# Optimization experiments

Hardware: AMD Instinct MI355X
Metric: run time of the kernel (lower is better)

Reference implementation:

```python
import jax, jax.numpy as jnp
import numpy as np

M, H, D, P = 16, 32, 128, 8192
N = H * D


def setup_inputs() -> dict:
    key = jax.random.key(0)
    k1, k2, k3, k4, k5, k6 = jax.random.split(key, 6)
    X = jax.random.normal(k1, (M, N), dtype=jnp.float32)
    # small init scale keeps the module's naive (unstabilized) exp-softmax finite
    Wq = jax.random.normal(k2, (N, N), dtype=jnp.float32) * 0.02
    Wk = jax.random.normal(k3, (N, N), dtype=jnp.float32) * 0.02
    Wv = jax.random.normal(k4, (N, N), dtype=jnp.float32) * 0.02
    cache_K = jax.random.normal(k5, (H, P, D), dtype=jnp.float32) * 0.05
    cache_V = jax.random.normal(k6, (H, P, D), dtype=jnp.float32)
    return {"X": X, "Wq": Wq, "Wk": Wk, "Wv": Wv,
            "cache_K": cache_K, "cache_V": cache_V}


def reference(X, Wq, Wk, Wv, cache_K, cache_V):
    m, n = X.shape                      # [M, N]
    h, p, d = cache_K.shape             # [H, P, D]
    # RMSNorm (no learned scale, matches (X*X).sum / N)
    x2 = jnp.sum(X * X, axis=1)
    x_norm = X / jnp.sqrt(x2 / n)[:, None]
    # QKV projections (nn.Linear, no bias -> x @ W.T)
    q = (x_norm @ Wq.T).reshape(m, h, d).transpose(1, 0, 2)   # [H, M, D]
    k = (x_norm @ Wk.T).reshape(m, h, d).transpose(1, 0, 2)   # [H, M, D]
    v = (x_norm @ Wv.T).reshape(m, h, d).transpose(1, 0, 2)   # [H, M, D]
    # append to cache
    ck = jnp.concatenate([cache_K, k], axis=1)                # [H, P+M, D]
    cv = jnp.concatenate([cache_V, v], axis=1)                # [H, P+M, D]
    # scores (no 1/sqrt(D) scaling in the original) + naive softmax
    c = jnp.einsum('hmd,hpd->hmp', q, ck)                     # [H, M, P+M]
    c_exp = jnp.exp(c)
    c_div = c_exp / jnp.sum(c_exp, axis=2, keepdims=True)
    o = jnp.einsum('hmp,hpd->hmd', c_div, cv)                 # [H, M, D]
    return o.transpose(1, 0, 2).reshape(m, n)                 # [M, N]
```

## Files before the change

### kernel.cpp

```cpp
#include <hip/hip_runtime.h>

#define NN 4096
#define HH 32
#define DD 128
#define MM 16
#define PP 8192

__device__ __forceinline__ float4 ld4(const float* p) { return *(const float4*)p; }
__device__ __forceinline__ float dot4f(float4 a, float4 b) {
  return a.x * b.x + a.y * b.y + a.z * b.z + a.w * b.w;
}
__device__ __forceinline__ void accumv(float* o, float e, float4 a, float4 b,
                                       float4 c, float4 d) {
  o[0] += e * a.x;  o[1] += e * a.y;  o[2] += e * a.z;  o[3] += e * a.w;
  o[4] += e * b.x;  o[5] += e * b.y;  o[6] += e * b.z;  o[7] += e * b.w;
  o[8] += e * c.x;  o[9] += e * c.y;  o[10] += e * c.z; o[11] += e * c.w;
  o[12] += e * d.x; o[13] += e * d.y; o[14] += e * d.z; o[15] += e * d.w;
}

__global__ void k1_rms(const float* __restrict__ X, float* __restrict__ inv) {
  const int m = blockIdx.x;
  const int tid = threadIdx.x;
  float s = 0.f;
#pragma unroll
  for (int i = 0; i < 16; ++i) {
    float v = X[(size_t)m * NN + i * 256 + tid];
    s += v * v;
  }
#pragma unroll
  for (int off = 1; off < 64; off <<= 1) s += __shfl_xor(s, off, 64);
  __shared__ float red[4];
  if ((tid & 63) == 0) red[tid >> 6] = s;
  __syncthreads();
  if (tid == 0) {
    float t = red[0] + red[1] + red[2] + red[3];
    inv[m] = rsqrtf(t * (1.0f / (float)NN));
  }
}

__global__ __launch_bounds__(256, 4) void k2_qkv(
    const float* __restrict__ X, const float* __restrict__ Wq,
    const float* __restrict__ Wk, const float* __restrict__ Wv,
    float* __restrict__ c_part) {
  __shared__ float lds_c[4][32][18];
  const int b = blockIdx.x;
  const int mat = b >> 9;
  const int rem = b & 511;
  const int qt = rem >> 7;
  const int jg = rem & 127;
  const float* W = (mat == 0) ? Wq : (mat == 1) ? Wk : Wv;
  const int tid = threadIdx.x;
  const int wave = tid >> 6;
  const int lane = tid & 63;
  const int m4 = lane & 3;
  const int g = lane >> 2;
  const int kbase = qt * 1024 + wave * 256 + g * 16;

  float4 xr[4][4];
#pragma unroll
  for (int mi = 0; mi < 4; ++mi) {
    const float* xp = X + (size_t)(mi * 4 + m4) * NN + kbase;
#pragma unroll
    for (int j = 0; j < 4; ++j) xr[mi][j] = ld4(xp + j * 4);
  }

  const int j0 = jg * 32;
  for (int grp = 0; grp < 8; ++grp) {
    float acc[4][4];
#pragma unroll
    for (int r = 0; r < 4; ++r)
#pragma unroll
      for (int mi = 0; mi < 4; ++mi) acc[r][mi] = 0.f;
#pragma unroll
    for (int r = 0; r < 4; ++r) {
      const float* wp = W + (size_t)(j0 + grp * 4 + r) * NN + kbase;
      float4 w0 = ld4(wp);
      float4 w1 = ld4(wp + 4);
      float4 w2 = ld4(wp + 8);
      float4 w3 = ld4(wp + 12);
#pragma unroll
      for (int mi = 0; mi < 4; ++mi)
        acc[r][mi] = acc[r][mi] + dot4f(xr[mi][0], w0) + dot4f(xr[mi][1], w1) +
                     dot4f(xr[mi][2], w2) + dot4f(xr[mi][3], w3);
    }
#pragma unroll
    for (int off = 4; off < 64; off <<= 1)
#pragma unroll
      for (int r = 0; r < 4; ++r)
#pragma unroll
        for (int mi = 0; mi < 4; ++mi)
          acc[r][mi] += __shfl_xor(acc[r][mi], off, 64);
    if (g == 0) {
#pragma unroll
      for (int r = 0; r < 4; ++r)
#pragma unroll
        for (int mi = 0; mi < 4; ++mi)
          lds_c[wave][grp * 4 + r][mi * 4 + m4] = acc[r][mi];
    }
  }
  __syncthreads();
#pragma unroll
  for (int i = 0; i < 2; ++i) {
    const int idx = i * 256 + tid;
    const int j = idx & 31;
    const int m = idx >> 5;
    float s = lds_c[0][j][m] + lds_c[1][j][m] + lds_c[2][j][m] + lds_c[3][j][m];
    c_part[(((size_t)(mat * 4 + qt) * 16 + m) << 12) + (j0 + j)] = s;
  }
}

__global__ __launch_bounds__(256, 4) void k3_attn(
    const float* __restrict__ cK, const float* __restrict__ cV,
    const float* __restrict__ c_part, const float* __restrict__ inv,
    float* __restrict__ o_part, float* __restrict__ denom_part) {
  const int chunk = blockIdx.x;
  const int h = blockIdx.y;
  const int tid = threadIdx.x;
  const int wave = tid >> 6;
  const int lane = tid & 63;
  const int m8 = lane & 7;
  const int g = lane >> 3;
  const int d0 = g * 16;

  float4 qa[4], qb[4];
  {
    float f[2][16];
#pragma unroll
    for (int mi = 0; mi < 2; ++mi)
#pragma unroll
      for (int j = 0; j < 16; ++j) f[mi][j] = 0.f;
#pragma unroll
    for (int qt = 0; qt < 4; ++qt) {
#pragma unroll
      for (int mi = 0; mi < 2; ++mi) {
        const int m = mi * 8 + m8;
        const float* cp = c_part + (((size_t)(qt * 16 + m)) << 12) + h * DD + d0;
#pragma unroll
        for (int j = 0; j < 4; ++j) {
          float4 t = ld4(cp + j * 4);
          f[mi][j * 4 + 0] += t.x;
          f[mi][j * 4 + 1] += t.y;
          f[mi][j * 4 + 2] += t.z;
          f[mi][j * 4 + 3] += t.w;
        }
      }
    }
    const float i0 = inv[m8];
    const float i1 = inv[8 + m8];
#pragma unroll
    for (int j = 0; j < 4; ++j) {
      qa[j] = make_float4(f[0][j * 4] * i0, f[0][j * 4 + 1] * i0,
                          f[0][j * 4 + 2] * i0, f[0][j * 4 + 3] * i0);
      qb[j] = make_float4(f[1][j * 4] * i1, f[1][j * 4 + 1] * i1,
                          f[1][j * 4 + 2] * i1, f[1][j * 4 + 3] * i1);
    }
  }

  float oac0[16], oac1[16];
#pragma unroll
  for (int j = 0; j < 16; ++j) { oac0[j] = 0.f; oac1[j] = 0.f; }
  float den0 = 0.f, den1 = 0.f;

  if (chunk < 32) {
    const size_t rowb = ((size_t)h * PP + chunk * 256 + wave * 64) * DD;
    const float* kb = cK + rowb + d0;
    const float* vb = cV + rowb + d0;
#pragma unroll 2
    for (int pi = 0; pi < 64; ++pi) {
      const float* kp = kb + pi * DD;
      float4 k0 = ld4(kp), k1 = ld4(kp + 4), k2 = ld4(kp + 8), k3 = ld4(kp + 12);
      const float* vp = vb + pi * DD;
      float4 v0 = ld4(vp), v1 = ld4(vp + 4), v2 = ld4(vp + 8), v3 = ld4(vp + 12);
      float c0 = dot4f(qa[0], k0) + dot4f(qa[1], k1) + dot4f(qa[2], k2) + dot4f(qa[3], k3);
      float c1 = dot4f(qb[0], k0) + dot4f(qb[1], k1) + dot4f(qb[2], k2) + dot4f(qb[3], k3);
#pragma unroll
      for (int off = 8; off < 64; off <<= 1) {
        c0 += __shfl_xor(c0, off, 64);
        c1 += __shfl_xor(c1, off, 64);
      }
      float e0 = __expf(c0), e1 = __expf(c1);
      den0 += e0; den1 += e1;
      accumv(oac0, e0, v0, v1, v2, v3);
      accumv(oac1, e1, v0, v1, v2, v3);
    }
  } else {
#pragma unroll
    for (int pi = 0; pi < 4; ++pi) {
      const int p = wave * 4 + pi;
      float kk[16], vv[16];
#pragma unroll
      for (int j = 0; j < 16; ++j) { kk[j] = 0.f; vv[j] = 0.f; }
#pragma unroll
      for (int qt = 0; qt < 4; ++qt) {
        const float* cpk = c_part + (((size_t)((4 + qt) * 16 + p)) << 12) + h * DD + d0;
        const float* cpv = c_part + (((size_t)((8 + qt) * 16 + p)) << 12) + h * DD + d0;
#pragma unroll
        for (int j = 0; j < 4; ++j) {
          float4 tk = ld4(cpk + j * 4);
          float4 tv = ld4(cpv + j * 4);
          kk[j * 4 + 0] += tk.x; kk[j * 4 + 1] += tk.y;
          kk[j * 4 + 2] += tk.z; kk[j * 4 + 3] += tk.w;
          vv[j * 4 + 0] += tv.x; vv[j * 4 + 1] += tv.y;
          vv[j * 4 + 2] += tv.z; vv[j * 4 + 3] += tv.w;
        }
      }
      const float ip = inv[p];
      float4 k0 = make_float4(kk[0] * ip, kk[1] * ip, kk[2] * ip, kk[3] * ip);
      float4 k1 = make_float4(kk[4] * ip, kk[5] * ip, kk[6] * ip, kk[7] * ip);
      float4 k2 = make_float4(kk[8] * ip, kk[9] * ip, kk[10] * ip, kk[11] * ip);
      float4 k3 = make_float4(kk[12] * ip, kk[13] * ip, kk[14] * ip, kk[15] * ip);
      float4 v0 = make_float4(vv[0] * ip, vv[1] * ip, vv[2] * ip, vv[3] * ip);
      float4 v1 = make_float4(vv[4] * ip, vv[5] * ip, vv[6] * ip, vv[7] * ip);
      float4 v2 = make_float4(vv[8] * ip, vv[9] * ip, vv[10] * ip, vv[11] * ip);
      float4 v3 = make_float4(vv[12] * ip, vv[13] * ip, vv[14] * ip, vv[15] * ip);
      float c0 = dot4f(qa[0], k0) + dot4f(qa[1], k1) + dot4f(qa[2], k2) + dot4f(qa[3], k3);
      float c1 = dot4f(qb[0], k0) + dot4f(qb[1], k1) + dot4f(qb[2], k2) + dot4f(qb[3], k3);
#pragma unroll
      for (int off = 8; off < 64; off <<= 1) {
        c0 += __shfl_xor(c0, off, 64);
        c1 += __shfl_xor(c1, off, 64);
      }
      float e0 = __expf(c0), e1 = __expf(c1);
      den0 += e0; den1 += e1;
      accumv(oac0, e0, v0, v1, v2, v3);
      accumv(oac1, e1, v0, v1, v2, v3);
    }
  }

  const size_t wc = ((size_t)h * 33 + chunk) * 4 + wave;
  float* op0 = o_part + wc * 2048 + m8 * DD + d0;
  float* op1 = o_part + wc * 2048 + (8 + m8) * DD + d0;
#pragma unroll
  for (int j = 0; j < 4; ++j) {
    *(float4*)(op0 + j * 4) = make_float4(oac0[j * 4], oac0[j * 4 + 1],
                                          oac0[j * 4 + 2], oac0[j * 4 + 3]);
    *(float4*)(op1 + j * 4) = make_float4(oac1[j * 4], oac1[j * 4 + 1],
                                          oac1[j * 4 + 2], oac1[j * 4 + 3]);
  }
  if (g == 0) {
    denom_part[wc * 16 + m8] = den0;
    denom_part[wc * 16 + 8 + m8] = den1;
  }
}

__global__ void k4_final(const float* __restrict__ o_part,
                         const float* __restrict__ denom_part,
                         float* __restrict__ out) {
  const int b = blockIdx.x;
  const int h = b >> 3;
  const int sub = b & 7;
  const int tid = threadIdx.x;
  const int md = sub * 256 + tid;
  __shared__ float dinv[2];
  if (tid == 0 || tid == 128) {
    const int mm = md >> 7;
    float s = 0.f;
    for (int c = 0; c < 132; ++c)
      s += denom_part[((size_t)h * 132 + c) * 16 + mm];
    dinv[tid >> 7] = 1.0f / s;
  }
  __syncthreads();
  float s = 0.f;
  for (int c = 0; c < 132; ++c)
    s += o_part[((size_t)h * 132 + c) * 2048 + md];
  const int m = md >> 7;
  const int d = md & 127;
  out[(size_t)m * NN + h * DD + d] = s * dinv[tid >> 7];
}

extern "C" void kernel_launch(void* const* d_in, const int* in_sizes, int n_in,
                              void* d_out, int out_size, void* d_ws, size_t ws_size,
                              hipStream_t stream) {
  (void)in_sizes; (void)n_in; (void)out_size; (void)ws_size;
  const float* X  = (const float*)d_in[0];
  const float* Wq = (const float*)d_in[1];
  const float* Wk = (const float*)d_in[2];
  const float* Wv = (const float*)d_in[3];
  const float* cK = (const float*)d_in[4];
  const float* cV = (const float*)d_in[5];
  float* out = (float*)d_out;
  float* ws = (float*)d_ws;

  float* inv        = ws;
  float* c_part     = ws + 16;
  float* o_part     = c_part + 786432;
  float* denom_part = o_part + 8650752;

  k1_rms<<<16, 256, 0, stream>>>(X, inv);
  k2_qkv<<<1536, 256, 0, stream>>>(X, Wq, Wk, Wv, c_part);
  k3_attn<<<dim3(33, 32), 256, 0, stream>>>(cK, cV, c_part, inv, o_part, denom_part);
  k4_final<<<256, 256, 0, stream>>>(o_part, denom_part, out);
}
```

Baseline: 537.1 us.

## Stage weights and KV cache through double-buffered LDS, add QKV combine kernel

The QKV projection now cooperatively loads contiguous 4-row weight tiles into double-buffered shared memory with register prefetch, instead of each lane issuing strided global loads. A new combine kernel sums the split-K partials and applies the RMS scale once, so the attention kernel no longer recomputes q/k/v from partials in every block. Attention is regridded to 512 blocks of 512 positions each, with K/V tiles staged through double-buffered LDS and the new-token tail folded into one block per head. The cost is an extra launch, more barriers and lower occupancy from the larger LDS footprint.

```diff
diff --git a/kernel.cpp b/kernel.cpp
--- a/kernel.cpp
+++ b/kernel.cpp
@@ -6,16 +6,9 @@
 #define MM 16
 #define PP 8192
 
-__device__ __forceinline__ float4 ld4(const float* p) { return *(const float4*)p; }
+__device__ __forceinline__ float4 ld4(const float* p) { return *(const float4*)(p); }
 __device__ __forceinline__ float dot4f(float4 a, float4 b) {
   return a.x * b.x + a.y * b.y + a.z * b.z + a.w * b.w;
-}
-__device__ __forceinline__ void accumv(float* o, float e, float4 a, float4 b,
-                                       float4 c, float4 d) {
-  o[0] += e * a.x;  o[1] += e * a.y;  o[2] += e * a.z;  o[3] += e * a.w;
-  o[4] += e * b.x;  o[5] += e * b.y;  o[6] += e * b.z;  o[7] += e * b.w;
-  o[8] += e * c.x;  o[9] += e * c.y;  o[10] += e * c.z; o[11] += e * c.w;
-  o[12] += e * d.x; o[13] += e * d.y; o[14] += e * d.z; o[15] += e * d.w;
 }
 
 __global__ void k1_rms(const float* __restrict__ X, float* __restrict__ inv) {
@@ -38,23 +31,24 @@
   }
 }
 
-__global__ __launch_bounds__(256, 4) void k2_qkv(
+__global__ __launch_bounds__(256, 3) void k2_qkv(
     const float* __restrict__ X, const float* __restrict__ Wq,
     const float* __restrict__ Wk, const float* __restrict__ Wv,
     float* __restrict__ c_part) {
-  __shared__ float lds_c[4][32][18];
+  __shared__ float wt[2][4][1024];
+  __shared__ float lds_c[4][32][17];
   const int b = blockIdx.x;
   const int mat = b >> 9;
-  const int rem = b & 511;
-  const int qt = rem >> 7;
-  const int jg = rem & 127;
+  const int qt = (b >> 7) & 3;
+  const int rb = b & 127;
   const float* W = (mat == 0) ? Wq : (mat == 1) ? Wk : Wv;
   const int tid = threadIdx.x;
   const int wave = tid >> 6;
   const int lane = tid & 63;
   const int m4 = lane & 3;
   const int g = lane >> 2;
-  const int kbase = qt * 1024 + wave * 256 + g * 16;
+  const int kwin = wave * 256 + g * 16;
+  const int kbase = qt * 1024 + kwin;
 
   float4 xr[4][4];
 #pragma unroll
@@ -64,8 +58,28 @@
     for (int j = 0; j < 4; ++j) xr[mi][j] = ld4(xp + j * 4);
   }
 
-  const int j0 = jg * 32;
-  for (int grp = 0; grp < 8; ++grp) {
+  const float* Wbase = W + (size_t)(rb * 32) * NN + qt * 1024;
+  float4 rw[4];
+#pragma unroll
+  for (int i = 0; i < 4; ++i) {
+    const int id = tid + i * 256;
+    rw[i] = *((const float4*)(Wbase + (size_t)(id >> 8) * NN) + (id & 255));
+  }
+
+  for (int tt = 0; tt < 8; ++tt) {
+    __syncthreads();
+#pragma unroll
+    for (int i = 0; i < 4; ++i)
+      ((float4*)wt[tt & 1])[tid + i * 256] = rw[i];
+    __syncthreads();
+    if (tt < 7) {
+      const float* Wn = Wbase + (size_t)((tt + 1) * 4) * NN;
+#pragma unroll
+      for (int i = 0; i < 4; ++i) {
+        const int id = tid + i * 256;
+        rw[i] = *((const float4*)(Wn + (size_t)(id >> 8) * NN) + (id & 255));
+      }
+    }
     float acc[4][4];
 #pragma unroll
     for (int r = 0; r < 4; ++r)
@@ -73,15 +87,12 @@
       for (int mi = 0; mi < 4; ++mi) acc[r][mi] = 0.f;
 #pragma unroll
     for (int r = 0; r < 4; ++r) {
-      const float* wp = W + (size_t)(j0 + grp * 4 + r) * NN + kbase;
-      float4 w0 = ld4(wp);
-      float4 w1 = ld4(wp + 4);
-      float4 w2 = ld4(wp + 8);
-      float4 w3 = ld4(wp + 12);
+      const float* wp = wt[tt & 1][r] + kwin;
+      float4 w0 = ld4(wp), w1 = ld4(wp + 4), w2 = ld4(wp + 8), w3 = ld4(wp + 12);
 #pragma unroll
       for (int mi = 0; mi < 4; ++mi)
-        acc[r][mi] = acc[r][mi] + dot4f(xr[mi][0], w0) + dot4f(xr[mi][1], w1) +
-                     dot4f(xr[mi][2], w2) + dot4f(xr[mi][3], w3);
+        acc[r][mi] += dot4f(xr[mi][0], w0) + dot4f(xr[mi][1], w1) +
+                      dot4f(xr[mi][2], w2) + dot4f(xr[mi][3], w3);
     }
 #pragma unroll
     for (int off = 4; off < 64; off <<= 1)
@@ -95,26 +106,44 @@
       for (int r = 0; r < 4; ++r)
 #pragma unroll
         for (int mi = 0; mi < 4; ++mi)
-          lds_c[wave][grp * 4 + r][mi * 4 + m4] = acc[r][mi];
+          lds_c[wave][tt * 4 + r][mi * 4 + m4] = acc[r][mi];
     }
   }
   __syncthreads();
 #pragma unroll
   for (int i = 0; i < 2; ++i) {
     const int idx = i * 256 + tid;
-    const int j = idx & 31;
-    const int m = idx >> 5;
-    float s = lds_c[0][j][m] + lds_c[1][j][m] + lds_c[2][j][m] + lds_c[3][j][m];
-    c_part[(((size_t)(mat * 4 + qt) * 16 + m) << 12) + (j0 + j)] = s;
-  }
-}
-
-__global__ __launch_bounds__(256, 4) void k3_attn(
+    const int l = idx >> 4;
+    const int m = idx & 15;
+    float s = lds_c[0][l][m] + lds_c[1][l][m] + lds_c[2][l][m] + lds_c[3][l][m];
+    c_part[(((size_t)(mat * 4 + qt) * 16 + m) << 12) + (rb * 32 + l)] = s;
+  }
+}
+
+__global__ void k2b_combine(const float* __restrict__ c_part,
+                            const float* __restrict__ inv,
+                            float* __restrict__ qkv) {
+  const int t = blockIdx.x * 256 + threadIdx.x;
+  const int mat = t >> 16;
+  const int r = t & 65535;
+  const int m = r >> 12;
+  const int j = r & 4095;
+  float s = 0.f;
+#pragma unroll
+  for (int qt = 0; qt < 4; ++qt)
+    s += c_part[(((size_t)(mat * 4 + qt) * 16 + m) << 12) + j];
+  qkv[(((size_t)(mat * 16 + m)) << 12) + j] = s * inv[m];
+}
+
+__global__ __launch_bounds__(256, 2) void k3_attn(
     const float* __restrict__ cK, const float* __restrict__ cV,
-    const float* __restrict__ c_part, const float* __restrict__ inv,
-    float* __restrict__ o_part, float* __restrict__ denom_part) {
-  const int chunk = blockIdx.x;
-  const int h = blockIdx.y;
+    const float* __restrict__ qkv, float* __restrict__ o_part,
+    float* __restrict__ den_part) {
+  __shared__ float sK[2][4096];
+  __shared__ float sV[2][4096];
+  const int b = blockIdx.x;
+  const int h = b >> 4;
+  const int seg = b & 15;
   const int tid = threadIdx.x;
   const int wave = tid >> 6;
   const int lane = tid & 63;
@@ -122,57 +151,50 @@
   const int g = lane >> 3;
   const int d0 = g * 16;
 
-  float4 qa[4], qb[4];
+  float4 q0[4], q1[4];
   {
-    float f[2][16];
-#pragma unroll
-    for (int mi = 0; mi < 2; ++mi)
-#pragma unroll
-      for (int j = 0; j < 16; ++j) f[mi][j] = 0.f;
-#pragma unroll
-    for (int qt = 0; qt < 4; ++qt) {
-#pragma unroll
-      for (int mi = 0; mi < 2; ++mi) {
-        const int m = mi * 8 + m8;
-        const float* cp = c_part + (((size_t)(qt * 16 + m)) << 12) + h * DD + d0;
-#pragma unroll
-        for (int j = 0; j < 4; ++j) {
-          float4 t = ld4(cp + j * 4);
-          f[mi][j * 4 + 0] += t.x;
-          f[mi][j * 4 + 1] += t.y;
-          f[mi][j * 4 + 2] += t.z;
-          f[mi][j * 4 + 3] += t.w;
-        }
+    const float* qa = qkv + (size_t)m8 * NN + h * DD + d0;
+    const float* qb = qkv + (size_t)(m8 + 8) * NN + h * DD + d0;
+#pragma unroll
+    for (int j = 0; j < 4; ++j) { q0[j] = ld4(qa + j * 4); q1[j] = ld4(qb + j * 4); }
+  }
+  float o0[16], o1[16];
+#pragma unroll
+  for (int j = 0; j < 16; ++j) { o0[j] = 0.f; o1[j] = 0.f; }
+  float den0 = 0.f, den1 = 0.f;
+
+  const float4* gK = (const float4*)(cK + ((size_t)h * PP + seg * 512) * DD);
+  const float4* gV = (const float4*)(cV + ((size_t)h * PP + seg * 512) * DD);
+
+  float4 rk[4], rv[4];
+#pragma unroll
+  for (int i = 0; i < 4; ++i) { rk[i] = gK[tid + i * 256]; rv[i] = gV[tid + i * 256]; }
+
+  for (int t = 0; t < 16; ++t) {
+    __syncthreads();
+#pragma unroll
+    for (int i = 0; i < 4; ++i) {
+      ((float4*)sK[t & 1])[tid + i * 256] = rk[i];
+      ((float4*)sV[t & 1])[tid + i * 256] = rv[i];
+    }
+    __syncthreads();
+    if (t < 15) {
+      const int base = (t + 1) * 1024;
+#pragma unroll
+      for (int i = 0; i < 4; ++i) {
+        rk[i] = gK[base + tid + i * 256];
+        rv[i] = gV[base + tid + i * 256];
       }
     }
-    const float i0 = inv[m8];
-    const float i1 = inv[8 + m8];
-#pragma unroll
-    for (int j = 0; j < 4; ++j) {
-      qa[j] = make_float4(f[0][j * 4] * i0, f[0][j * 4 + 1] * i0,
-                          f[0][j * 4 + 2] * i0, f[0][j * 4 + 3] * i0);
-      qb[j] = make_float4(f[1][j * 4] * i1, f[1][j * 4 + 1] * i1,
-                          f[1][j * 4 + 2] * i1, f[1][j * 4 + 3] * i1);
-    }
-  }
-
-  float oac0[16], oac1[16];
-#pragma unroll
-  for (int j = 0; j < 16; ++j) { oac0[j] = 0.f; oac1[j] = 0.f; }
-  float den0 = 0.f, den1 = 0.f;
-
-  if (chunk < 32) {
-    const size_t rowb = ((size_t)h * PP + chunk * 256 + wave * 64) * DD;
-    const float* kb = cK + rowb + d0;
-    const float* vb = cV + rowb + d0;
-#pragma unroll 2
-    for (int pi = 0; pi < 64; ++pi) {
-      const float* kp = kb + pi * DD;
+    const float* bK = sK[t & 1];
+    const float* bV = sV[t & 1];
+#pragma unroll
+    for (int pi = 0; pi < 8; ++pi) {
+      const int p = wave * 8 + pi;
+      const float* kp = bK + p * DD + d0;
       float4 k0 = ld4(kp), k1 = ld4(kp + 4), k2 = ld4(kp + 8), k3 = ld4(kp + 12);
-      const float* vp = vb + pi * DD;
-      float4 v0 = ld4(vp), v1 = ld4(vp + 4), v2 = ld4(vp + 8), v3 = ld4(vp + 12);
-      float c0 = dot4f(qa[0], k0) + dot4f(qa[1], k1) + dot4f(qa[2], k2) + dot4f(qa[3], k3);
-      float c1 = dot4f(qb[0], k0) + dot4f(qb[1], k1) + dot4f(qb[2], k2) + dot4f(qb[3], k3);
+      float c0 = dot4f(q0[0], k0) + dot4f(q0[1], k1) + dot4f(q0[2], k2) + dot4f(q0[3], k3);
+      float c1 = dot4f(q1[0], k0) + dot4f(q1[1], k1) + dot4f(q1[2], k2) + dot4f(q1[3], k3);
 #pragma unroll
       for (int off = 8; off < 64; off <<= 1) {
         c0 += __shfl_xor(c0, off, 64);
@@ -180,41 +202,39 @@
       }
       float e0 = __expf(c0), e1 = __expf(c1);
       den0 += e0; den1 += e1;
-      accumv(oac0, e0, v0, v1, v2, v3);
-      accumv(oac1, e1, v0, v1, v2, v3);
-    }
-  } else {
+      const float* vp = bV + p * DD + d0;
+      float4 v0 = ld4(vp), v1 = ld4(vp + 4), v2 = ld4(vp + 8), v3 = ld4(vp + 12);
+      o0[0] += e0 * v0.x;  o0[1] += e0 * v0.y;  o0[2] += e0 * v0.z;  o0[3] += e0 * v0.w;
+      o0[4] += e0 * v1.x;  o0[5] += e0 * v1.y;  o0[6] += e0 * v1.z;  o0[7] += e0 * v1.w;
+      o0[8] += e0 * v2.x;  o0[9] += e0 * v2.y;  o0[10] += e0 * v2.z; o0[11] += e0 * v2.w;
+      o0[12] += e0 * v3.x; o0[13] += e0 * v3.y; o0[14] += e0 * v3.z; o0[15] += e0 * v3.w;
+      o1[0] += e1 * v0.x;  o1[1] += e1 * v0.y;  o1[2] += e1 * v0.z;  o1[3] += e1 * v0.w;
+      o1[4] += e1 * v1.x;  o1[5] += e1 * v1.y;  o1[6] += e1 * v1.z;  o1[7] += e1 * v1.w;
+      o1[8] += e1 * v2.x;  o1[9] += e1 * v2.y;  o1[10] += e1 * v2.z; o1[11] += e1 * v2.w;
+      o1[12] += e1 * v3.x; o1[13] += e1 * v3.y; o1[14] += e1 * v3.z; o1[15] += e1 * v3.w;
+    }
+  }
+
+  if (seg == (h & 15)) {
+    __syncthreads();
+    const int r0 = tid >> 5;
+    const int c = tid & 31;
+#pragma unroll
+    for (int rr = 0; rr < 2; ++rr) {
+      const int p = rr * 8 + r0;
+      ((float4*)sK[0])[p * 32 + c] =
+          *((const float4*)(qkv + (size_t)(16 + p) * NN + h * DD) + c);
+      ((float4*)sV[0])[p * 32 + c] =
+          *((const float4*)(qkv + (size_t)(32 + p) * NN + h * DD) + c);
+    }
+    __syncthreads();
 #pragma unroll
     for (int pi = 0; pi < 4; ++pi) {
       const int p = wave * 4 + pi;
-      float kk[16], vv[16];
-#pragma unroll
-      for (int j = 0; j < 16; ++j) { kk[j] = 0.f; vv[j] = 0.f; }
-#pragma unroll
-      for (int qt = 0; qt < 4; ++qt) {
-        const float* cpk = c_part + (((size_t)((4 + qt) * 16 + p)) << 12) + h * DD + d0;
-        const float* cpv = c_part + (((size_t)((8 + qt) * 16 + p)) << 12) + h * DD + d0;
-#pragma unroll
-        for (int j = 0; j < 4; ++j) {
-          float4 tk = ld4(cpk + j * 4);
-          float4 tv = ld4(cpv + j * 4);
-          kk[j * 4 + 0] += tk.x; kk[j * 4 + 1] += tk.y;
-          kk[j * 4 + 2] += tk.z; kk[j * 4 + 3] += tk.w;
-          vv[j * 4 + 0] += tv.x; vv[j * 4 + 1] += tv.y;
-          vv[j * 4 + 2] += tv.z; vv[j * 4 + 3] += tv.w;
-        }
-      }
-      const float ip = inv[p];
-      float4 k0 = make_float4(kk[0] * ip, kk[1] * ip, kk[2] * ip, kk[3] * ip);
-      float4 k1 = make_float4(kk[4] * ip, kk[5] * ip, kk[6] * ip, kk[7] * ip);
-      float4 k2 = make_float4(kk[8] * ip, kk[9] * ip, kk[10] * ip, kk[11] * ip);
-      float4 k3 = make_float4(kk[12] * ip, kk[13] * ip, kk[14] * ip, kk[15] * ip);
-      float4 v0 = make_float4(vv[0] * ip, vv[1] * ip, vv[2] * ip, vv[3] * ip);
-      float4 v1 = make_float4(vv[4] * ip, vv[5] * ip, vv[6] * ip, vv[7] * ip);
-      float4 v2 = make_float4(vv[8] * ip, vv[9] * ip, vv[10] * ip, vv[11] * ip);
-      float4 v3 = make_float4(vv[12] * ip, vv[13] * ip, vv[14] * ip, vv[15] * ip);
-      float c0 = dot4f(qa[0], k0) + dot4f(qa[1], k1) + dot4f(qa[2], k2) + dot4f(qa[3], k3);
-      float c1 = dot4f(qb[0], k0) + dot4f(qb[1], k1) + dot4f(qb[2], k2) + dot4f(qb[3], k3);
+      const float* kp = sK[0] + p * DD + d0;
+      float4 k0 = ld4(kp), k1 = ld4(kp + 4), k2 = ld4(kp + 8), k3 = ld4(kp + 12);
+      float c0 = dot4f(q0[0], k0) + dot4f(q0[1], k1) + dot4f(q0[2], k2) + dot4f(q0[3], k3);
+      float c1 = dot4f(q1[0], k0) + dot4f(q1[1], k1) + dot4f(q1[2], k2) + dot4f(q1[3], k3);
 #pragma unroll
       for (int off = 8; off < 64; off <<= 1) {
         c0 += __shfl_xor(c0, off, 64);
@@ -222,50 +242,52 @@
       }
       float e0 = __expf(c0), e1 = __expf(c1);
       den0 += e0; den1 += e1;
-      accumv(oac0, e0, v0, v1, v2, v3);
-      accumv(oac1, e1, v0, v1, v2, v3);
-    }
-  }
-
-  const size_t wc = ((size_t)h * 33 + chunk) * 4 + wave;
-  float* op0 = o_part + wc * 2048 + m8 * DD + d0;
-  float* op1 = o_part + wc * 2048 + (8 + m8) * DD + d0;
+      const float* vp = sV[0] + p * DD + d0;
+      float4 v0 = ld4(vp), v1 = ld4(vp + 4), v2 = ld4(vp + 8), v3 = ld4(vp + 12);
+      o0[0] += e0 * v0.x;  o0[1] += e0 * v0.y;  o0[2] += e0 * v0.z;  o0[3] += e0 * v0.w;
+      o0[4] += e0 * v1.x;  o0[5] += e0 * v1.y;  o0[6] += e0 * v1.z;  o0[7] += e0 * v1.w;
+      o0[8] += e0 * v2.x;  o0[9] += e0 * v2.y;  o0[10] += e0 * v2.z; o0[11] += e0 * v2.w;
+      o0[12] += e0 * v3.x; o0[13] += e0 * v3.y; o0[14] += e0 * v3.z; o0[15] += e0 * v3.w;
+      o1[0] += e1 * v0.x;  o1[1] += e1 * v0.y;  o1[2] += e1 * v0.z;  o1[3] += e1 * v0.w;
+      o1[4] += e1 * v1.x;  o1[5] += e1 * v1.y;  o1[6] += e1 * v1.z;  o1[7] += e1 * v1.w;
+      o1[8] += e1 * v2.x;  o1[9] += e1 * v2.y;  o1[10] += e1 * v2.z; o1[11] += e1 * v2.w;
+      o1[12] += e1 * v3.x; o1[13] += e1 * v3.y; o1[14] += e1 * v3.z; o1[15] += e1 * v3.w;
+    }
+  }
+
+  float* op = o_part + ((size_t)b * 4 + wave) * 2048;
 #pragma unroll
   for (int j = 0; j < 4; ++j) {
-    *(float4*)(op0 + j * 4) = make_float4(oac0[j * 4], oac0[j * 4 + 1],
-                                          oac0[j * 4 + 2], oac0[j * 4 + 3]);
-    *(float4*)(op1 + j * 4) = make_float4(oac1[j * 4], oac1[j * 4 + 1],
-                                          oac1[j * 4 + 2], oac1[j * 4 + 3]);
+    *(float4*)(op + m8 * DD + d0 + j * 4) =
+        make_float4(o0[j * 4], o0[j * 4 + 1], o0[j * 4 + 2], o0[j * 4 + 3]);
+    *(float4*)(op + (m8 + 8) * DD + d0 + j * 4) =
+        make_float4(o1[j * 4], o1[j * 4 + 1], o1[j * 4 + 2], o1[j * 4 + 3]);
   }
   if (g == 0) {
-    denom_part[wc * 16 + m8] = den0;
-    denom_part[wc * 16 + 8 + m8] = den1;
+    den_part[((size_t)b * 4 + wave) * 16 + m8] = den0;
+    den_part[((size_t)b * 4 + wave) * 16 + 8 + m8] = den1;
   }
 }
 
 __global__ void k4_final(const float* __restrict__ o_part,
-                         const float* __restrict__ denom_part,
+                         const float* __restrict__ den_part,
                          float* __restrict__ out) {
   const int b = blockIdx.x;
   const int h = b >> 3;
-  const int sub = b & 7;
   const int tid = threadIdx.x;
-  const int md = sub * 256 + tid;
-  __shared__ float dinv[2];
-  if (tid == 0 || tid == 128) {
-    const int mm = md >> 7;
+  const int idx = (b & 7) * 256 + tid;
+  __shared__ float dinv[16];
+  if (tid < 16) {
     float s = 0.f;
-    for (int c = 0; c < 132; ++c)
-      s += denom_part[((size_t)h * 132 + c) * 16 + mm];
-    dinv[tid >> 7] = 1.0f / s;
+    for (int j = 0; j < 64; ++j) s += den_part[(size_t)h * 1024 + j * 16 + tid];
+    dinv[tid] = 1.0f / s;
   }
   __syncthreads();
   float s = 0.f;
-  for (int c = 0; c < 132; ++c)
-    s += o_part[((size_t)h * 132 + c) * 2048 + md];
-  const int m = md >> 7;
-  const int d = md & 127;
-  out[(size_t)m * NN + h * DD + d] = s * dinv[tid >> 7];
+  for (int j = 0; j < 64; ++j) s += o_part[(size_t)h * 131072 + j * 2048 + idx];
+  const int m = idx >> 7;
+  const int d = idx & 127;
+  out[(size_t)m * NN + h * DD + d] = s * dinv[m];
 }
 
 extern "C" void kernel_launch(void* const* d_in, const int* in_sizes, int n_in,
@@ -281,13 +303,15 @@
   float* out = (float*)d_out;
   float* ws = (float*)d_ws;
 
-  float* inv        = ws;
-  float* c_part     = ws + 16;
-  float* o_part     = c_part + 786432;
-  float* denom_part = o_part + 8650752;
+  float* inv      = ws;
+  float* c_part   = ws + 16;
+  float* qkv      = c_part + 786432;
+  float* o_part   = qkv + 196608;
+  float* den_part = o_part + 4194304;
 
   k1_rms<<<16, 256, 0, stream>>>(X, inv);
   k2_qkv<<<1536, 256, 0, stream>>>(X, Wq, Wk, Wv, c_part);
-  k3_attn<<<dim3(33, 32), 256, 0, stream>>>(cK, cV, c_part, inv, o_part, denom_part);
-  k4_final<<<256, 256, 0, stream>>>(o_part, denom_part, out);
-}
+  k2b_combine<<<768, 256, 0, stream>>>(c_part, inv, qkv);
+  k3_attn<<<dim3(512), 256, 0, stream>>>(cK, cV, qkv, o_part, den_part);
+  k4_final<<<256, 256, 0, stream>>>(o_part, den_part, out);
+}
```

Result: faster. 478.8 us (-10.9%).
